# Optimization experiments

Hardware: AMD Instinct MI355X
Metric: run time of the kernel (lower is better)

Reference implementation:

```python
import jax, jax.numpy as jnp
import numpy as np

N_NODES = 50000
N_EDGES = 800000
F = 128
LN_EPS = 1e-5


def _sage_conv(h, src, dst, Wl, bl, Wr, n_nodes):
    # PyG SAGEConv (aggr='mean', root_weight=True):
    #   out_i = lin_l(mean_{j->i} h_j) + lin_r(h_i)
    msg = h[src]  # [E, F] irregular gather
    s = jax.ops.segment_sum(msg, dst, num_segments=n_nodes)  # [N, F]
    deg = jax.ops.segment_sum(jnp.ones((src.shape[0],), h.dtype), dst,
                              num_segments=n_nodes)  # [N]
    mean = s / jnp.maximum(deg, 1.0)[:, None]
    return mean @ Wl.T + bl + h @ Wr.T


def _graph_layernorm(h, w, b):
    # PyG LayerNorm mode='graph', batch=None: normalize over ALL entries,
    # eps added to std, then per-channel affine.
    m = h.mean()
    std = jnp.sqrt(jnp.mean((h - m) ** 2))
    return (h - m) / (std + LN_EPS) * w + b


def _prelu(h, w):
    # nn.PReLU(1): single shared slope
    return jnp.where(h >= 0, h, w * h)


def setup_inputs() -> dict:
    key = jax.random.key(0)
    ks = jax.random.split(key, 12)
    sc = 1.0 / np.sqrt(F)
    x = jax.random.normal(ks[0], (N_NODES, F), dtype=jnp.float32)
    edge_index = jax.random.randint(ks[1], (2, N_EDGES), 0, N_NODES, dtype=jnp.int64)
    return {
        "x": x,
        "edge_index": edge_index,
        "Wl0": jax.random.uniform(ks[2], (F, F), jnp.float32, -sc, sc),
        "bl0": jnp.zeros((F,), jnp.float32),
        "Wr0": jax.random.uniform(ks[3], (F, F), jnp.float32, -sc, sc),
        "ln_w0": jnp.ones((F,), jnp.float32),
        "ln_b0": jnp.zeros((F,), jnp.float32),
        "pw0": jnp.full((1,), 0.25, jnp.float32),
        "skipW0": jax.random.uniform(ks[4], (F, F), jnp.float32, -sc, sc),
        "Wl1": jax.random.uniform(ks[5], (F, F), jnp.float32, -sc, sc),
        "bl1": jnp.zeros((F,), jnp.float32),
        "Wr1": jax.random.uniform(ks[6], (F, F), jnp.float32, -sc, sc),
        "ln_w1": jnp.ones((F,), jnp.float32),
        "ln_b1": jnp.zeros((F,), jnp.float32),
        "pw1": jnp.full((1,), 0.25, jnp.float32),
    }


def reference(x, edge_index, Wl0, bl0, Wr0, ln_w0, ln_b0, pw0, skipW0,
              Wl1, bl1, Wr1, ln_w1, ln_b1, pw1):
    src, dst = edge_index[0], edge_index[1]
    n = x.shape[0]
    # layer 0: h = x
    h = _sage_conv(x, src, dst, Wl0, bl0, Wr0, n)
    h = _graph_layernorm(h, ln_w0, ln_b0)
    h1 = _prelu(h, pw0)
    # layer 1: h = skip(x) + h1
    h = x @ skipW0.T + h1
    h = _sage_conv(h, src, dst, Wl1, bl1, Wr1, n)
    h = _graph_layernorm(h, ln_w1, ln_b1)
    h = _prelu(h, pw1)
    return h
```

## Files before the change

kernel.cpp:

```cpp
#include <hip/hip_runtime.h>

#define LN_EPS 1e-5f
#define BUCKCAP 2048
#define PCHUNK 6656
#define PK 13

typedef short bf16x8 __attribute__((ext_vector_type(8)));
typedef float f32x4  __attribute__((ext_vector_type(4)));

static __device__ __forceinline__ float4 ld4(const float* p){ return *(const float4*)p; }
static __device__ __forceinline__ uint f2bf1(float f){
  uint u = __float_as_uint(f);
  return (u + 0x7fffu + ((u >> 16) & 1u)) >> 16;
}
static __device__ __forceinline__ float bf2f(uint lo16){ return __uint_as_float(lo16 << 16); }

__global__ __launch_bounds__(256) void prep_kernel(
    const float* __restrict__ x, ushort* __restrict__ x16, int nxb, int n8,
    const float* __restrict__ s0, const float* __restrict__ s1,
    const float* __restrict__ s2, const float* __restrict__ s3,
    const float* __restrict__ s4, ushort* __restrict__ wdst,
    double* __restrict__ stats, int* __restrict__ bcnt, int* __restrict__ cnts){
  int bid = blockIdx.x, tid = threadIdx.x;
  if (bid < nxb){
    int i = bid*256 + tid;
    if (i >= n8) return;
    float4 a = ld4(x + (size_t)i*8);
    float4 b = ld4(x + (size_t)i*8 + 4);
    uint4 o;
    o.x = f2bf1(a.x) | (f2bf1(a.y) << 16);
    o.y = f2bf1(a.z) | (f2bf1(a.w) << 16);
    o.z = f2bf1(b.x) | (f2bf1(b.y) << 16);
    o.w = f2bf1(b.z) | (f2bf1(b.w) << 16);
    *(uint4*)(x16 + (size_t)i*8) = o;
  } else if (bid < nxb + 40){
    int i = (bid - nxb)*256 + tid;
    int m = i >> 11;
    int o = (i & 2047) * 8;
    const float* s = (m == 0) ? s0 : (m == 1) ? s1 : (m == 2) ? s2 : (m == 3) ? s3 : s4;
    float4 a = ld4(s + o);
    float4 b = ld4(s + o + 4);
    uint4 v;
    v.x = f2bf1(a.x) | (f2bf1(a.y) << 16);
    v.y = f2bf1(a.z) | (f2bf1(a.w) << 16);
    v.z = f2bf1(b.x) | (f2bf1(b.y) << 16);
    v.w = f2bf1(b.z) | (f2bf1(b.w) << 16);
    *(uint4*)(wdst + (size_t)m*16384 + o) = v;
  } else {
    bcnt[tid] = 0; bcnt[tid + 256] = 0; bcnt[tid + 512] = 0; bcnt[tid + 768] = 0;
    if (tid < 4) stats[tid] = 0.0;
    if (tid < 2) cnts[tid] = 0;
  }
}

__global__ __launch_bounds__(512) void partition_kernel(
    const int* __restrict__ ei, int E,
    int* __restrict__ bucket_count, uint* __restrict__ ebuf){
  __shared__ int hist[1024];
  __shared__ int base[1024];
  __shared__ int cur[1024];
  __shared__ int anyv;
  const int tid = threadIdx.x;
  const int lo = blockIdx.x * PCHUNK;
  const int hi = min(lo + PCHUNK, E);
  hist[tid] = 0; hist[tid + 512] = 0;
  if (tid == 0) anyv = 0;
  __syncthreads();
  int nz = 0;
  for (int i = tid; i < 1024; i += 512) nz |= (ei[2*i+1] != 0);
  if (nz) atomicOr(&anyv, 1);
  __syncthreads();
  const int fmt = anyv;

  uint pd[PK];
  #pragma unroll
  for (int k = 0; k < PK; k++){
    int e = lo + tid + k*512;
    uint v = 0xffffffffu;
    if (e < hi){
      int s, d;
      if (fmt){ s = ei[e]; d = ei[E + e]; }
      else    { s = ei[2*e]; d = ei[2*(E + e)]; }
      v = ((uint)d << 16) | (uint)s;
      atomicAdd(&hist[v >> 22], 1);
    }
    pd[k] = v;
  }
  __syncthreads();
  #pragma unroll
  for (int t0 = 0; t0 < 2; t0++){
    int t = tid + t0*512;
    int h = hist[t];
    base[t] = (h > 0) ? atomicAdd(&bucket_count[t], h) : 0;
    cur[t] = 0;
  }
  __syncthreads();
  #pragma unroll
  for (int k = 0; k < PK; k++){
    int e = lo + tid + k*512;
    if (e < hi){
      uint v = pd[k];
      int b = v >> 22;
      int pos = base[b] + atomicAdd(&cur[b], 1);
      if (pos < BUCKCAP) ebuf[(size_t)b*BUCKCAP + pos] = v;
    }
  }
}

__global__ __launch_bounds__(512) void bucket_aggregate(const ushort* __restrict__ h,
    const uint* __restrict__ ebuf, const int* __restrict__ bucket_count,
    ushort* __restrict__ outmean, int N){
  __shared__ ushort ssrc[BUCKCAP];
  __shared__ int lcnt[64], lofs[64], lcur[64];
  const int tid = threadIdx.x;
  const int b = blockIdx.x;
  const int n0 = b << 6;
  const uint* eb = ebuf + (size_t)b*BUCKCAP;
  const int cnt = min(bucket_count[b], BUCKCAP);

  if (tid < 64) lcnt[tid] = 0;
  __syncthreads();
  for (int e = tid; e < cnt; e += 512)
    atomicAdd(&lcnt[(eb[e] >> 16) & 63], 1);
  __syncthreads();
  if (tid < 64){
    int v = lcnt[tid];
    int s = v;
    #pragma unroll
    for (int off = 1; off < 64; off <<= 1){
      int u = __shfl_up(s, off);
      if (tid >= off) s += u;
    }
    lofs[tid] = s - v;
    lcur[tid] = s - v;
  }
  __syncthreads();
  for (int e = tid; e < cnt; e += 512){
    uint v = eb[e];
    int pos = atomicAdd(&lcur[(v >> 16) & 63], 1);
    ssrc[pos] = (ushort)(v & 0xffffu);
  }
  __syncthreads();

  const int wv = tid >> 6, lane = tid & 63;
  const uint* hp = (const uint*)h;
  uint* op = (uint*)outmean;
  #pragma unroll 1
  for (int i = 0; i < 8; i++){
    int j = wv*8 + i;
    int node = n0 + j;
    if (node >= N) break;
    int start = lofs[j];
    int d = lcnt[j];
    float ax = 0.f, ay = 0.f;
    int e = 0;
    for (; e + 8 <= d; e += 8){
      uint v0 = hp[(size_t)ssrc[start+e+0]*64 + lane];
      uint v1 = hp[(size_t)ssrc[start+e+1]*64 + lane];
      uint v2 = hp[(size_t)ssrc[start+e+2]*64 + lane];
      uint v3 = hp[(size_t)ssrc[start+e+3]*64 + lane];
      uint v4 = hp[(size_t)ssrc[start+e+4]*64 + lane];
      uint v5 = hp[(size_t)ssrc[start+e+5]*64 + lane];
      uint v6 = hp[(size_t)ssrc[start+e+6]*64 + lane];
      uint v7 = hp[(size_t)ssrc[start+e+7]*64 + lane];
      ax += bf2f(v0 & 0xffffu) + bf2f(v1 & 0xffffu) + bf2f(v2 & 0xffffu) + bf2f(v3 & 0xffffu)
          + bf2f(v4 & 0xffffu) + bf2f(v5 & 0xffffu) + bf2f(v6 & 0xffffu) + bf2f(v7 & 0xffffu);
      ay += bf2f(v0 >> 16) + bf2f(v1 >> 16) + bf2f(v2 >> 16) + bf2f(v3 >> 16)
          + bf2f(v4 >> 16) + bf2f(v5 >> 16) + bf2f(v6 >> 16) + bf2f(v7 >> 16);
    }
    for (; e < d; e++){
      uint v = hp[(size_t)ssrc[start+e]*64 + lane];
      ax += bf2f(v & 0xffffu);
      ay += bf2f(v >> 16);
    }
    float inv = 1.f / fmaxf((float)d, 1.f);
    op[(size_t)node*64 + lane] = f2bf1(ax*inv) | (f2bf1(ay*inv) << 16);
  }
}

static __device__ __forceinline__ void grid_barrier(int* cnt, int nblocks, int tid){
  __syncthreads();
  if (tid == 0){
    __threadfence();
    atomicAdd(cnt, 1);
    while (__hip_atomic_load(cnt, __ATOMIC_ACQUIRE, __HIP_MEMORY_SCOPE_AGENT) < nblocks){
      __builtin_amdgcn_s_sleep(8);
    }
    __threadfence();
  }
  __syncthreads();
}

__global__ __launch_bounds__(256, 2) void fused_layer0(
    const ushort* __restrict__ A1 , const ushort* __restrict__ A2 ,
    const ushort* __restrict__ Wl, const ushort* __restrict__ Wr,
    const ushort* __restrict__ Wsk,
    const float* __restrict__ bias,
    const float* __restrict__ lnw, const float* __restrict__ lnb,
    const float* __restrict__ pw,
    ushort* __restrict__ outb, int N, double inv_cnt,
    double* __restrict__ stats, int* __restrict__ bar){
  const int tid  = threadIdx.x;
  const int lane = tid & 63;
  const int wv   = tid >> 6;
  const int r0   = blockIdx.x*128 + wv*32;
  const int lrow = lane & 15;
  const int lk   = (lane >> 4) * 8;

  f32x4 accD[2][8] = {};
  f32x4 accS[2][8] = {};

  #pragma unroll
  for (int ks = 0; ks < 4; ks++){
    const int kb = ks*32 + lk;
    bf16x8 a1[2], a2[2];
    #pragma unroll
    for (int m = 0; m < 2; m++){
      int r = r0 + m*16 + lrow;
      if (r > N-1) r = N-1;
      a1[m] = *(const bf16x8*)(A1 + (size_t)r*128 + kb);
      a2[m] = *(const bf16x8*)(A2 + (size_t)r*128 + kb);
    }
    #pragma unroll
    for (int n = 0; n < 8; n++){
      const int c = n*16 + lrow;
      bf16x8 bl = *(const bf16x8*)(Wl  + c*128 + kb);
      bf16x8 br = *(const bf16x8*)(Wr  + c*128 + kb);
      bf16x8 bs = *(const bf16x8*)(Wsk + c*128 + kb);
      #pragma unroll
      for (int m = 0; m < 2; m++){
        accD[m][n] = __builtin_amdgcn_mfma_f32_16x16x32_bf16(a1[m], bl, accD[m][n], 0, 0, 0);
        accD[m][n] = __builtin_amdgcn_mfma_f32_16x16x32_bf16(a2[m], br, accD[m][n], 0, 0, 0);
        accS[m][n] = __builtin_amdgcn_mfma_f32_16x16x32_bf16(a2[m], bs, accS[m][n], 0, 0, 0);
      }
    }
  }

  float bn[8], wn[8], bb[8];
  #pragma unroll
  for (int n = 0; n < 8; n++){
    bn[n] = bias[n*16 + lrow];
    wn[n] = lnw[n*16 + lrow];
    bb[n] = lnb[n*16 + lrow];
  }

  double ls1 = 0.0, ls2 = 0.0;
  const int rb = (lane >> 4) * 4;
  #pragma unroll
  for (int m = 0; m < 2; m++){
    #pragma unroll
    for (int j = 0; j < 4; j++){
      int r = r0 + m*16 + rb + j;
      if (r < N){
        #pragma unroll
        for (int n = 0; n < 8; n++){
          float v = accD[m][n][j] + bn[n];
          ls1 += (double)v;
          ls2 += (double)v * (double)v;
        }
      }
    }
  }
  #pragma unroll
  for (int off = 32; off > 0; off >>= 1){
    ls1 += __shfl_down(ls1, off);
    ls2 += __shfl_down(ls2, off);
  }
  __shared__ double red[8];
  if (lane == 0){ red[wv*2] = ls1; red[wv*2+1] = ls2; }
  __syncthreads();
  if (tid == 0){
    atomicAdd(&stats[0], red[0]+red[2]+red[4]+red[6]);
    atomicAdd(&stats[1], red[1]+red[3]+red[5]+red[7]);
  }

  grid_barrier(bar, gridDim.x, tid);

  double s1 = __hip_atomic_load(&stats[0], __ATOMIC_RELAXED, __HIP_MEMORY_SCOPE_AGENT);
  double s2 = __hip_atomic_load(&stats[1], __ATOMIC_RELAXED, __HIP_MEMORY_SCOPE_AGENT);
  double md = s1 * inv_cnt;
  double var = s2 * inv_cnt - md*md;
  float mean = (float)md;
  float rstd = 1.f / ((float)sqrt(fmax(var, 0.0)) + LN_EPS);
  float slope = pw[0];

  #pragma unroll
  for (int m = 0; m < 2; m++){
    #pragma unroll
    for (int j = 0; j < 4; j++){
      int r = r0 + m*16 + rb + j;
      if (r < N){
        #pragma unroll
        for (int n = 0; n < 8; n++){
          float t = accD[m][n][j] + bn[n];
          float l = (t - mean)*rstd*wn[n] + bb[n];
          l = (l >= 0.f) ? l : slope*l;
          float v = accS[m][n][j] + l;
          outb[(size_t)r*128 + n*16 + lrow] = (ushort)f2bf1(v);
        }
      }
    }
  }
}

__global__ __launch_bounds__(256, 2) void fused_layer1(
    const ushort* __restrict__ A1 , const ushort* __restrict__ A2 ,
    const ushort* __restrict__ Wl, const ushort* __restrict__ Wr,
    const float* __restrict__ bias,
    const float* __restrict__ lnw, const float* __restrict__ lnb,
    const float* __restrict__ pw,
    float* __restrict__ out, int N, double inv_cnt,
    double* __restrict__ stats, int* __restrict__ bar){
  const int tid  = threadIdx.x;
  const int lane = tid & 63;
  const int wv   = tid >> 6;
  const int r0   = blockIdx.x*128 + wv*32;
  const int lrow = lane & 15;
  const int lk   = (lane >> 4) * 8;

  f32x4 accD[2][8] = {};

  #pragma unroll
  for (int ks = 0; ks < 4; ks++){
    const int kb = ks*32 + lk;
    bf16x8 a1[2], a2[2];
    #pragma unroll
    for (int m = 0; m < 2; m++){
      int r = r0 + m*16 + lrow;
      if (r > N-1) r = N-1;
      a1[m] = *(const bf16x8*)(A1 + (size_t)r*128 + kb);
      a2[m] = *(const bf16x8*)(A2 + (size_t)r*128 + kb);
    }
    #pragma unroll
    for (int n = 0; n < 8; n++){
      const int c = n*16 + lrow;
      bf16x8 bl = *(const bf16x8*)(Wl + c*128 + kb);
      bf16x8 br = *(const bf16x8*)(Wr + c*128 + kb);
      #pragma unroll
      for (int m = 0; m < 2; m++){
        accD[m][n] = __builtin_amdgcn_mfma_f32_16x16x32_bf16(a1[m], bl, accD[m][n], 0, 0, 0);
        accD[m][n] = __builtin_amdgcn_mfma_f32_16x16x32_bf16(a2[m], br, accD[m][n], 0, 0, 0);
      }
    }
  }

  float bn[8], wn[8], bb[8];
  #pragma unroll
  for (int n = 0; n < 8; n++){
    bn[n] = bias[n*16 + lrow];
    wn[n] = lnw[n*16 + lrow];
    bb[n] = lnb[n*16 + lrow];
  }

  double ls1 = 0.0, ls2 = 0.0;
  const int rb = (lane >> 4) * 4;
  #pragma unroll
  for (int m = 0; m < 2; m++){
    #pragma unroll
    for (int j = 0; j < 4; j++){
      int r = r0 + m*16 + rb + j;
      if (r < N){
        #pragma unroll
        for (int n = 0; n < 8; n++){
          float v = accD[m][n][j] + bn[n];
          ls1 += (double)v;
          ls2 += (double)v * (double)v;
        }
      }
    }
  }
  #pragma unroll
  for (int off = 32; off > 0; off >>= 1){
    ls1 += __shfl_down(ls1, off);
    ls2 += __shfl_down(ls2, off);
  }
  __shared__ double red[8];
  if (lane == 0){ red[wv*2] = ls1; red[wv*2+1] = ls2; }
  __syncthreads();
  if (tid == 0){
    atomicAdd(&stats[0], red[0]+red[2]+red[4]+red[6]);
    atomicAdd(&stats[1], red[1]+red[3]+red[5]+red[7]);
  }

  grid_barrier(bar, gridDim.x, tid);

  double s1 = __hip_atomic_load(&stats[0], __ATOMIC_RELAXED, __HIP_MEMORY_SCOPE_AGENT);
  double s2 = __hip_atomic_load(&stats[1], __ATOMIC_RELAXED, __HIP_MEMORY_SCOPE_AGENT);
  double md = s1 * inv_cnt;
  double var = s2 * inv_cnt - md*md;
  float mean = (float)md;
  float rstd = 1.f / ((float)sqrt(fmax(var, 0.0)) + LN_EPS);
  float slope = pw[0];

  #pragma unroll
  for (int m = 0; m < 2; m++){
    #pragma unroll
    for (int j = 0; j < 4; j++){
      int r = r0 + m*16 + rb + j;
      if (r < N){
        #pragma unroll
        for (int n = 0; n < 8; n++){
          float t = accD[m][n][j] + bn[n];
          float l = (t - mean)*rstd*wn[n] + bb[n];
          l = (l >= 0.f) ? l : slope*l;
          out[(size_t)r*128 + n*16 + lrow] = l;
        }
      }
    }
  }
}

extern "C" void kernel_launch(void* const* d_in, const int* in_sizes, int n_in,
                              void* d_out, int out_size, void* d_ws, size_t ws_size,
                              hipStream_t stream){
  const float* x    = (const float*)d_in[0];
  const int*   ei   = (const int*)d_in[1];
  const float* Wl0  = (const float*)d_in[2];
  const float* bl0  = (const float*)d_in[3];
  const float* Wr0  = (const float*)d_in[4];
  const float* lnw0 = (const float*)d_in[5];
  const float* lnb0 = (const float*)d_in[6];
  const float* pw0  = (const float*)d_in[7];
  const float* skW  = (const float*)d_in[8];
  const float* Wl1  = (const float*)d_in[9];
  const float* bl1  = (const float*)d_in[10];
  const float* Wr1  = (const float*)d_in[11];
  const float* lnw1 = (const float*)d_in[12];
  const float* lnb1 = (const float*)d_in[13];
  const float* pw1  = (const float*)d_in[14];

  const int N = in_sizes[0] / 128;
  const int E = in_sizes[1] / 2;

  char* p = (char*)d_ws;
  auto carve = [&](size_t bytes)->char*{
    char* r = p;
    p += (bytes + 255) & ~(size_t)255;
    return r;
  };
  double* stats   = (double*)carve(4*sizeof(double));
  int*    cnts    = (int*)carve(2*sizeof(int));
  int*    bcnt    = (int*)carve((size_t)1024*4);
  uint*   ebuf    = (uint*)carve((size_t)1024*BUCKCAP*4);
  ushort* x16     = (ushort*)carve((size_t)N*128*2);
  ushort* mean16  = (ushort*)carve((size_t)N*128*2);
  ushort* hskip16 = (ushort*)carve((size_t)N*128*2);
  ushort* wbuf    = (ushort*)carve((size_t)5*16384*2);

  ushort* Wl0_16 = wbuf;
  ushort* Wr0_16 = wbuf + 16384;
  ushort* skW_16 = wbuf + 32768;
  ushort* Wl1_16 = wbuf + 49152;
  ushort* Wr1_16 = wbuf + 65536;

  const int n8  = N*16;
  const int nxb = (n8 + 255)/256;
  const int nbuck = (N + 63) >> 6;
  const int pb = (E + PCHUNK - 1) / PCHUNK;
  const int gb = (N + 127)/128;
  const double inv_cnt = 1.0 / ((double)N * 128.0);

  prep_kernel<<<nxb + 40 + 1, 256, 0, stream>>>(x, x16, nxb, n8,
      Wl0, Wr0, skW, Wl1, Wr1, wbuf, stats, bcnt, cnts);
  partition_kernel<<<pb, 512, 0, stream>>>(ei, E, bcnt, ebuf);

  bucket_aggregate<<<nbuck, 512, 0, stream>>>(x16, ebuf, bcnt, mean16, N);
  fused_layer0<<<gb, 256, 0, stream>>>(mean16, x16, Wl0_16, Wr0_16, skW_16,
      bl0, lnw0, lnb0, pw0, hskip16, N, inv_cnt, stats, &cnts[0]);
  bucket_aggregate<<<nbuck, 512, 0, stream>>>(hskip16, ebuf, bcnt, mean16, N);
  fused_layer1<<<gb, 256, 0, stream>>>(mean16, hskip16, Wl1_16, Wr1_16,
      bl1, lnw1, lnb1, pw1, (float*)d_out, N, inv_cnt, stats + 2, &cnts[1]);
}
```

Before: 312.0 us.

## Fuse neighbor aggregation into GEMM and split LayerNorm into separate elementwise pass

```diff
diff --git a/kernel.cpp b/kernel.cpp
--- a/kernel.cpp
+++ b/kernel.cpp
@@ -20,7 +20,7 @@
     const float* __restrict__ s0, const float* __restrict__ s1,
     const float* __restrict__ s2, const float* __restrict__ s3,
     const float* __restrict__ s4, ushort* __restrict__ wdst,
-    double* __restrict__ stats, int* __restrict__ bcnt, int* __restrict__ cnts){
+    double* __restrict__ stats, int* __restrict__ bcnt){
   int bid = blockIdx.x, tid = threadIdx.x;
   if (bid < nxb){
     int i = bid*256 + tid;
@@ -49,7 +49,6 @@
   } else {
     bcnt[tid] = 0; bcnt[tid + 256] = 0; bcnt[tid + 512] = 0; bcnt[tid + 768] = 0;
     if (tid < 4) stats[tid] = 0.0;
-    if (tid < 2) cnts[tid] = 0;
   }
 }
 
@@ -107,11 +106,20 @@
   }
 }
 
-__global__ __launch_bounds__(512) void bucket_aggregate(const ushort* __restrict__ h,
+template<int NMAT>
+__global__ __launch_bounds__(512, 4) void agg_gemm(
+    const ushort* __restrict__ h,
     const uint* __restrict__ ebuf, const int* __restrict__ bucket_count,
-    ushort* __restrict__ outmean, int N){
+    const ushort* __restrict__ Wl, const ushort* __restrict__ Wr,
+    const ushort* __restrict__ Wsk,
+    const float* __restrict__ bias,
+    ushort* __restrict__ tout, ushort* __restrict__ skout,
+    int N, double* __restrict__ stats){
   __shared__ ushort ssrc[BUCKCAP];
   __shared__ int lcnt[64], lofs[64], lcur[64];
+  __shared__ ushort Am[64][136];
+  __shared__ double red[16];
+
   const int tid = threadIdx.x;
   const int b = blockIdx.x;
   const int n0 = b << 6;
@@ -144,120 +152,86 @@
 
   const int wv = tid >> 6, lane = tid & 63;
   const uint* hp = (const uint*)h;
-  uint* op = (uint*)outmean;
   #pragma unroll 1
   for (int i = 0; i < 8; i++){
     int j = wv*8 + i;
     int node = n0 + j;
-    if (node >= N) break;
-    int start = lofs[j];
-    int d = lcnt[j];
-    float ax = 0.f, ay = 0.f;
-    int e = 0;
-    for (; e + 8 <= d; e += 8){
-      uint v0 = hp[(size_t)ssrc[start+e+0]*64 + lane];
-      uint v1 = hp[(size_t)ssrc[start+e+1]*64 + lane];
-      uint v2 = hp[(size_t)ssrc[start+e+2]*64 + lane];
-      uint v3 = hp[(size_t)ssrc[start+e+3]*64 + lane];
-      uint v4 = hp[(size_t)ssrc[start+e+4]*64 + lane];
-      uint v5 = hp[(size_t)ssrc[start+e+5]*64 + lane];
-      uint v6 = hp[(size_t)ssrc[start+e+6]*64 + lane];
-      uint v7 = hp[(size_t)ssrc[start+e+7]*64 + lane];
-      ax += bf2f(v0 & 0xffffu) + bf2f(v1 & 0xffffu) + bf2f(v2 & 0xffffu) + bf2f(v3 & 0xffffu)
-          + bf2f(v4 & 0xffffu) + bf2f(v5 & 0xffffu) + bf2f(v6 & 0xffffu) + bf2f(v7 & 0xffffu);
-      ay += bf2f(v0 >> 16) + bf2f(v1 >> 16) + bf2f(v2 >> 16) + bf2f(v3 >> 16)
-          + bf2f(v4 >> 16) + bf2f(v5 >> 16) + bf2f(v6 >> 16) + bf2f(v7 >> 16);
-    }
-    for (; e < d; e++){
-      uint v = hp[(size_t)ssrc[start+e]*64 + lane];
-      ax += bf2f(v & 0xffffu);
-      ay += bf2f(v >> 16);
-    }
-    float inv = 1.f / fmaxf((float)d, 1.f);
-    op[(size_t)node*64 + lane] = f2bf1(ax*inv) | (f2bf1(ay*inv) << 16);
-  }
-}
-
-static __device__ __forceinline__ void grid_barrier(int* cnt, int nblocks, int tid){
-  __syncthreads();
-  if (tid == 0){
-    __threadfence();
-    atomicAdd(cnt, 1);
-    while (__hip_atomic_load(cnt, __ATOMIC_ACQUIRE, __HIP_MEMORY_SCOPE_AGENT) < nblocks){
-      __builtin_amdgcn_s_sleep(8);
-    }
-    __threadfence();
-  }
-  __syncthreads();
-}
-
-__global__ __launch_bounds__(256, 2) void fused_layer0(
-    const ushort* __restrict__ A1 , const ushort* __restrict__ A2 ,
-    const ushort* __restrict__ Wl, const ushort* __restrict__ Wr,
-    const ushort* __restrict__ Wsk,
-    const float* __restrict__ bias,
-    const float* __restrict__ lnw, const float* __restrict__ lnb,
-    const float* __restrict__ pw,
-    ushort* __restrict__ outb, int N, double inv_cnt,
-    double* __restrict__ stats, int* __restrict__ bar){
-  const int tid  = threadIdx.x;
-  const int lane = tid & 63;
-  const int wv   = tid >> 6;
-  const int r0   = blockIdx.x*128 + wv*32;
-  const int lrow = lane & 15;
-  const int lk   = (lane >> 4) * 8;
-
-  f32x4 accD[2][8] = {};
-  f32x4 accS[2][8] = {};
+    uint packed = 0;
+    if (node < N){
+      int start = lofs[j];
+      int d = lcnt[j];
+      float ax = 0.f, ay = 0.f;
+      int e = 0;
+      for (; e + 8 <= d; e += 8){
+        uint v0 = hp[(size_t)ssrc[start+e+0]*64 + lane];
+        uint v1 = hp[(size_t)ssrc[start+e+1]*64 + lane];
+        uint v2 = hp[(size_t)ssrc[start+e+2]*64 + lane];
+        uint v3 = hp[(size_t)ssrc[start+e+3]*64 + lane];
+        uint v4 = hp[(size_t)ssrc[start+e+4]*64 + lane];
+        uint v5 = hp[(size_t)ssrc[start+e+5]*64 + lane];
+        uint v6 = hp[(size_t)ssrc[start+e+6]*64 + lane];
+        uint v7 = hp[(size_t)ssrc[start+e+7]*64 + lane];
+        ax += bf2f(v0 & 0xffffu) + bf2f(v1 & 0xffffu) + bf2f(v2 & 0xffffu) + bf2f(v3 & 0xffffu)
+            + bf2f(v4 & 0xffffu) + bf2f(v5 & 0xffffu) + bf2f(v6 & 0xffffu) + bf2f(v7 & 0xffffu);
+        ay += bf2f(v0 >> 16) + bf2f(v1 >> 16) + bf2f(v2 >> 16) + bf2f(v3 >> 16)
+            + bf2f(v4 >> 16) + bf2f(v5 >> 16) + bf2f(v6 >> 16) + bf2f(v7 >> 16);
+      }
+      for (; e < d; e++){
+        uint v = hp[(size_t)ssrc[start+e]*64 + lane];
+        ax += bf2f(v & 0xffffu);
+        ay += bf2f(v >> 16);
+      }
+      float inv = 1.f / fmaxf((float)d, 1.f);
+      packed = f2bf1(ax*inv) | (f2bf1(ay*inv) << 16);
+    }
+    *(uint*)&Am[j][lane*2] = packed;
+  }
+  __syncthreads();
+
+  const int wrow  = (wv & 3) * 16;
+  const int chalf = (wv >> 2) * 64;
+  const int lrow  = lane & 15;
+  const int lk8   = (lane >> 4) * 8;
+
+  f32x4 accT[4] = {};
+  f32x4 accS[4] = {};
 
   #pragma unroll
   for (int ks = 0; ks < 4; ks++){
-    const int kb = ks*32 + lk;
-    bf16x8 a1[2], a2[2];
+    const int kb = ks*32 + lk8;
+    bf16x8 a1 = *(const bf16x8*)&Am[wrow + lrow][kb];
+    int r = n0 + wrow + lrow; if (r > N-1) r = N-1;
+    bf16x8 a2 = *(const bf16x8*)(h + (size_t)r*128 + kb);
     #pragma unroll
-    for (int m = 0; m < 2; m++){
-      int r = r0 + m*16 + lrow;
-      if (r > N-1) r = N-1;
-      a1[m] = *(const bf16x8*)(A1 + (size_t)r*128 + kb);
-      a2[m] = *(const bf16x8*)(A2 + (size_t)r*128 + kb);
-    }
-    #pragma unroll
-    for (int n = 0; n < 8; n++){
-      const int c = n*16 + lrow;
-      bf16x8 bl = *(const bf16x8*)(Wl  + c*128 + kb);
-      bf16x8 br = *(const bf16x8*)(Wr  + c*128 + kb);
-      bf16x8 bs = *(const bf16x8*)(Wsk + c*128 + kb);
-      #pragma unroll
-      for (int m = 0; m < 2; m++){
-        accD[m][n] = __builtin_amdgcn_mfma_f32_16x16x32_bf16(a1[m], bl, accD[m][n], 0, 0, 0);
-        accD[m][n] = __builtin_amdgcn_mfma_f32_16x16x32_bf16(a2[m], br, accD[m][n], 0, 0, 0);
-        accS[m][n] = __builtin_amdgcn_mfma_f32_16x16x32_bf16(a2[m], bs, accS[m][n], 0, 0, 0);
+    for (int n = 0; n < 4; n++){
+      const int c = chalf + n*16 + lrow;
+      bf16x8 bl = *(const bf16x8*)(Wl + c*128 + kb);
+      bf16x8 br = *(const bf16x8*)(Wr + c*128 + kb);
+      accT[n] = __builtin_amdgcn_mfma_f32_16x16x32_bf16(a1, bl, accT[n], 0, 0, 0);
+      accT[n] = __builtin_amdgcn_mfma_f32_16x16x32_bf16(a2, br, accT[n], 0, 0, 0);
+      if (NMAT == 3){
+        bf16x8 bs = *(const bf16x8*)(Wsk + c*128 + kb);
+        accS[n] = __builtin_amdgcn_mfma_f32_16x16x32_bf16(a2, bs, accS[n], 0, 0, 0);
       }
     }
-  }
-
-  float bn[8], wn[8], bb[8];
-  #pragma unroll
-  for (int n = 0; n < 8; n++){
-    bn[n] = bias[n*16 + lrow];
-    wn[n] = lnw[n*16 + lrow];
-    bb[n] = lnb[n*16 + lrow];
   }
 
   double ls1 = 0.0, ls2 = 0.0;
   const int rb = (lane >> 4) * 4;
   #pragma unroll
-  for (int m = 0; m < 2; m++){
+  for (int n = 0; n < 4; n++){
+    const int col = chalf + n*16 + lrow;
+    float bnv = bias[col];
     #pragma unroll
     for (int j = 0; j < 4; j++){
-      int r = r0 + m*16 + rb + j;
+      int r = n0 + wrow + rb + j;
       if (r < N){
-        #pragma unroll
-        for (int n = 0; n < 8; n++){
-          float v = accD[m][n][j] + bn[n];
-          ls1 += (double)v;
-          ls2 += (double)v * (double)v;
-        }
+        float v = accT[n][j] + bnv;
+        tout[(size_t)r*128 + col] = (ushort)f2bf1(v);
+        ls1 += (double)v;
+        ls2 += (double)v * (double)v;
+        if (NMAT == 3)
+          skout[(size_t)r*128 + col] = (ushort)f2bf1(accS[n][j]);
       }
     }
   }
@@ -266,147 +240,65 @@
     ls1 += __shfl_down(ls1, off);
     ls2 += __shfl_down(ls2, off);
   }
-  __shared__ double red[8];
   if (lane == 0){ red[wv*2] = ls1; red[wv*2+1] = ls2; }
   __syncthreads();
   if (tid == 0){
-    atomicAdd(&stats[0], red[0]+red[2]+red[4]+red[6]);
-    atomicAdd(&stats[1], red[1]+red[3]+red[5]+red[7]);
-  }
-
-  grid_barrier(bar, gridDim.x, tid);
-
-  double s1 = __hip_atomic_load(&stats[0], __ATOMIC_RELAXED, __HIP_MEMORY_SCOPE_AGENT);
-  double s2 = __hip_atomic_load(&stats[1], __ATOMIC_RELAXED, __HIP_MEMORY_SCOPE_AGENT);
-  double md = s1 * inv_cnt;
-  double var = s2 * inv_cnt - md*md;
+    double s1 = red[0]+red[2]+red[4]+red[6]+red[8]+red[10]+red[12]+red[14];
+    atomicAdd(&stats[0], s1);
+  }
+  if (tid == 1){
+    double s2 = red[1]+red[3]+red[5]+red[7]+red[9]+red[11]+red[13]+red[15];
+    atomicAdd(&stats[1], s2);
+  }
+}
+
+__global__ __launch_bounds__(256) void ln_skip_kernel(
+    const ushort* __restrict__ t0, const ushort* __restrict__ sk,
+    const double* __restrict__ stats,
+    const float* __restrict__ lnw, const float* __restrict__ lnb,
+    const float* __restrict__ pw, ushort* __restrict__ outb,
+    int nu, double inv_cnt){
+  double md = stats[0] * inv_cnt;
+  double var = stats[1] * inv_cnt - md*md;
   float mean = (float)md;
   float rstd = 1.f / ((float)sqrt(fmax(var, 0.0)) + LN_EPS);
   float slope = pw[0];
-
-  #pragma unroll
-  for (int m = 0; m < 2; m++){
-    #pragma unroll
-    for (int j = 0; j < 4; j++){
-      int r = r0 + m*16 + rb + j;
-      if (r < N){
-        #pragma unroll
-        for (int n = 0; n < 8; n++){
-          float t = accD[m][n][j] + bn[n];
-          float l = (t - mean)*rstd*wn[n] + bb[n];
-          l = (l >= 0.f) ? l : slope*l;
-          float v = accS[m][n][j] + l;
-          outb[(size_t)r*128 + n*16 + lrow] = (ushort)f2bf1(v);
-        }
-      }
-    }
-  }
-}
-
-__global__ __launch_bounds__(256, 2) void fused_layer1(
-    const ushort* __restrict__ A1 , const ushort* __restrict__ A2 ,
-    const ushort* __restrict__ Wl, const ushort* __restrict__ Wr,
-    const float* __restrict__ bias,
+  const uint* tp = (const uint*)t0;
+  const uint* sp = (const uint*)sk;
+  uint* op = (uint*)outb;
+  for (int i = blockIdx.x*256 + threadIdx.x; i < nu; i += gridDim.x*256){
+    int c = (i & 63) * 2;
+    uint tv = tp[i], sv = sp[i];
+    float l0 = (bf2f(tv & 0xffffu) - mean)*rstd*lnw[c]   + lnb[c];
+    float l1 = (bf2f(tv >> 16)     - mean)*rstd*lnw[c+1] + lnb[c+1];
+    l0 = (l0 >= 0.f) ? l0 : slope*l0;
+    l1 = (l1 >= 0.f) ? l1 : slope*l1;
+    float v0 = bf2f(sv & 0xffffu) + l0;
+    float v1 = bf2f(sv >> 16)     + l1;
+    op[i] = f2bf1(v0) | (f2bf1(v1) << 16);
+  }
+}
+
+__global__ __launch_bounds__(256) void ln_out_kernel(
+    const ushort* __restrict__ t1, const double* __restrict__ stats,
     const float* __restrict__ lnw, const float* __restrict__ lnb,
-    const float* __restrict__ pw,
-    float* __restrict__ out, int N, double inv_cnt,
-    double* __restrict__ stats, int* __restrict__ bar){
-  const int tid  = threadIdx.x;
-  const int lane = tid & 63;
-  const int wv   = tid >> 6;
-  const int r0   = blockIdx.x*128 + wv*32;
-  const int lrow = lane & 15;
-  const int lk   = (lane >> 4) * 8;
-
-  f32x4 accD[2][8] = {};
-
-  #pragma unroll
-  for (int ks = 0; ks < 4; ks++){
-    const int kb = ks*32 + lk;
-    bf16x8 a1[2], a2[2];
-    #pragma unroll
-    for (int m = 0; m < 2; m++){
-      int r = r0 + m*16 + lrow;
-      if (r > N-1) r = N-1;
-      a1[m] = *(const bf16x8*)(A1 + (size_t)r*128 + kb);
-      a2[m] = *(const bf16x8*)(A2 + (size_t)r*128 + kb);
-    }
-    #pragma unroll
-    for (int n = 0; n < 8; n++){
-      const int c = n*16 + lrow;
-      bf16x8 bl = *(const bf16x8*)(Wl + c*128 + kb);
-      bf16x8 br = *(const bf16x8*)(Wr + c*128 + kb);
-      #pragma unroll
-      for (int m = 0; m < 2; m++){
-        accD[m][n] = __builtin_amdgcn_mfma_f32_16x16x32_bf16(a1[m], bl, accD[m][n], 0, 0, 0);
-        accD[m][n] = __builtin_amdgcn_mfma_f32_16x16x32_bf16(a2[m], br, accD[m][n], 0, 0, 0);
-      }
-    }
-  }
-
-  float bn[8], wn[8], bb[8];
-  #pragma unroll
-  for (int n = 0; n < 8; n++){
-    bn[n] = bias[n*16 + lrow];
-    wn[n] = lnw[n*16 + lrow];
-    bb[n] = lnb[n*16 + lrow];
-  }
-
-  double ls1 = 0.0, ls2 = 0.0;
-  const int rb = (lane >> 4) * 4;
-  #pragma unroll
-  for (int m = 0; m < 2; m++){
-    #pragma unroll
-    for (int j = 0; j < 4; j++){
-      int r = r0 + m*16 + rb + j;
-      if (r < N){
-        #pragma unroll
-        for (int n = 0; n < 8; n++){
-          float v = accD[m][n][j] + bn[n];
-          ls1 += (double)v;
-          ls2 += (double)v * (double)v;
-        }
-      }
-    }
-  }
-  #pragma unroll
-  for (int off = 32; off > 0; off >>= 1){
-    ls1 += __shfl_down(ls1, off);
-    ls2 += __shfl_down(ls2, off);
-  }
-  __shared__ double red[8];
-  if (lane == 0){ red[wv*2] = ls1; red[wv*2+1] = ls2; }
-  __syncthreads();
-  if (tid == 0){
-    atomicAdd(&stats[0], red[0]+red[2]+red[4]+red[6]);
-    atomicAdd(&stats[1], red[1]+red[3]+red[5]+red[7]);
-  }
-
-  grid_barrier(bar, gridDim.x, tid);
-
-  double s1 = __hip_atomic_load(&stats[0], __ATOMIC_RELAXED, __HIP_MEMORY_SCOPE_AGENT);
-  double s2 = __hip_atomic_load(&stats[1], __ATOMIC_RELAXED, __HIP_MEMORY_SCOPE_AGENT);
-  double md = s1 * inv_cnt;
-  double var = s2 * inv_cnt - md*md;
+    const float* __restrict__ pw, float* __restrict__ out,
+    int nu, double inv_cnt){
+  double md = stats[0] * inv_cnt;
+  double var = stats[1] * inv_cnt - md*md;
   float mean = (float)md;
   float rstd = 1.f / ((float)sqrt(fmax(var, 0.0)) + LN_EPS);
   float slope = pw[0];
-
-  #pragma unroll
-  for (int m = 0; m < 2; m++){
-    #pragma unroll
-    for (int j = 0; j < 4; j++){
-      int r = r0 + m*16 + rb + j;
-      if (r < N){
-        #pragma unroll
-        for (int n = 0; n < 8; n++){
-          float t = accD[m][n][j] + bn[n];
-          float l = (t - mean)*rstd*wn[n] + bb[n];
-          l = (l >= 0.f) ? l : slope*l;
-          out[(size_t)r*128 + n*16 + lrow] = l;
-        }
-      }
-    }
+  const uint* tp = (const uint*)t1;
+  for (int i = blockIdx.x*256 + threadIdx.x; i < nu; i += gridDim.x*256){
+    int c = (i & 63) * 2;
+    uint tv = tp[i];
+    float l0 = (bf2f(tv & 0xffffu) - mean)*rstd*lnw[c]   + lnb[c];
+    float l1 = (bf2f(tv >> 16)     - mean)*rstd*lnw[c+1] + lnb[c+1];
+    l0 = (l0 >= 0.f) ? l0 : slope*l0;
+    l1 = (l1 >= 0.f) ? l1 : slope*l1;
+    float2 v; v.x = l0; v.y = l1;
+    *(float2*)(out + (size_t)i*2) = v;
   }
 }
 
@@ -439,11 +331,11 @@
     return r;
   };
   double* stats   = (double*)carve(4*sizeof(double));
-  int*    cnts    = (int*)carve(2*sizeof(int));
   int*    bcnt    = (int*)carve((size_t)1024*4);
   uint*   ebuf    = (uint*)carve((size_t)1024*BUCKCAP*4);
   ushort* x16     = (ushort*)carve((size_t)N*128*2);
-  ushort* mean16  = (ushort*)carve((size_t)N*128*2);
+  ushort* tbuf16  = (ushort*)carve((size_t)N*128*2);
+  ushort* skbuf16 = (ushort*)carve((size_t)N*128*2);
   ushort* hskip16 = (ushort*)carve((size_t)N*128*2);
   ushort* wbuf    = (ushort*)carve((size_t)5*16384*2);
 
@@ -457,17 +349,20 @@
   const int nxb = (n8 + 255)/256;
   const int nbuck = (N + 63) >> 6;
   const int pb = (E + PCHUNK - 1) / PCHUNK;
-  const int gb = (N + 127)/128;
   const double inv_cnt = 1.0 / ((double)N * 128.0);
+  const int nu = N*64;
 
   prep_kernel<<<nxb + 40 + 1, 256, 0, stream>>>(x, x16, nxb, n8,
-      Wl0, Wr0, skW, Wl1, Wr1, wbuf, stats, bcnt, cnts);
+      Wl0, Wr0, skW, Wl1, Wr1, wbuf, stats, bcnt);
   partition_kernel<<<pb, 512, 0, stream>>>(ei, E, bcnt, ebuf);
 
-  bucket_aggregate<<<nbuck, 512, 0, stream>>>(x16, ebuf, bcnt, mean16, N);
-  fused_layer0<<<gb, 256, 0, stream>>>(mean16, x16, Wl0_16, Wr0_16, skW_16,
-      bl0, lnw0, lnb0, pw0, hskip16, N, inv_cnt, stats, &cnts[0]);
-  bucket_aggregate<<<nbuck, 512, 0, stream>>>(hskip16, ebuf, bcnt, mean16, N);
-  fused_layer1<<<gb, 256, 0, stream>>>(mean16, hskip16, Wl1_16, Wr1_16,
-      bl1, lnw1, lnb1, pw1, (float*)d_out, N, inv_cnt, stats + 2, &cnts[1]);
-}
+  agg_gemm<3><<<nbuck, 512, 0, stream>>>(x16, ebuf, bcnt,
+      Wl0_16, Wr0_16, skW_16, bl0, tbuf16, skbuf16, N, stats);
+  ln_skip_kernel<<<2048, 256, 0, stream>>>(tbuf16, skbuf16, stats,
+      lnw0, lnb0, pw0, hskip16, nu, inv_cnt);
+
+  agg_gemm<2><<<nbuck, 512, 0, stream>>>(hskip16, ebuf, bcnt,
+      Wl1_16, Wr1_16, nullptr, bl1, tbuf16, nullptr, N, stats + 2);
+  ln_out_kernel<<<2048, 256, 0, stream>>>(tbuf16, stats + 2,
+      lnw1, lnb1, pw1, (float*)d_out, nu, inv_cnt);
+}
```

Result: no change. 307.1 us (-1.6%).
